# Kernel optimization log

Hardware: AMD Instinct MI355X
Metric: run time of the kernel (lower is better)

The kernel has to match this reference:

```python
import jax, jax.numpy as jnp
import numpy as np

C, CB, W, N = 256, 64, 32, 16
F = CB * W  # 2048 lstm features


def setup_inputs() -> dict:
    key = jax.random.key(0)
    ks = jax.random.split(key, 8)
    sc = 1.0 / np.sqrt(F)  # matches torch LSTM uniform(-1/sqrt(H), 1/sqrt(H)) scale
    return {
        "latent": jax.random.normal(ks[0], (N, C, W, W), jnp.float32),
        "w_in": jax.random.normal(ks[1], (CB, C), jnp.float32) * 0.05,
        "b_in": jnp.zeros((CB,), jnp.float32),
        "w_ih0": jax.random.normal(ks[2], (4 * F, F), jnp.float32) * sc,
        "w_hh0": jax.random.normal(ks[3], (4 * F, F), jnp.float32) * sc,
        "b_ih0": jnp.zeros((4 * F,), jnp.float32),
        "b_hh0": jnp.zeros((4 * F,), jnp.float32),
        "w_ih1": jax.random.normal(ks[4], (4 * F, F), jnp.float32) * sc,
        "w_hh1": jax.random.normal(ks[5], (4 * F, F), jnp.float32) * sc,
        "b_ih1": jnp.zeros((4 * F,), jnp.float32),
        "b_hh1": jnp.zeros((4 * F,), jnp.float32),
        "w_out": jax.random.normal(ks[6], (C, CB), jnp.float32) * 0.05,
        "b_out": jnp.zeros((C,), jnp.float32),
    }


def _lstm_cell(xt, h, c, w_ih, w_hh, b):
    # torch gate order: i, f, g, o
    g = xt @ w_ih.T + h @ w_hh.T + b
    i, f, gg, o = jnp.split(g, 4, axis=-1)
    c = jax.nn.sigmoid(f) * c + jax.nn.sigmoid(i) * jnp.tanh(gg)
    h = jax.nn.sigmoid(o) * jnp.tanh(c)
    return h, c


def reference(latent, w_in, b_in, w_ih0, w_hh0, b_ih0, b_hh0,
              w_ih1, w_hh1, b_ih1, b_hh1, w_out, b_out):
    n, ch, w, hgt = latent.shape
    # bottleneck_in: 1x1 conv (Normalizer.NONE / Activation.NONE -> identity)
    x = jnp.einsum('nchw,oc->nohw', latent, w_in) + b_in[None, :, None, None]  # (N,CB,W,H)
    # (N,CB,W,H) -> (N,W,H,CB) -> (N,W,H*CB) -> (W,N,F)
    seq = x.transpose(0, 2, 3, 1).reshape(n, w, -1).transpose(1, 0, 2)

    b0 = b_ih0 + b_hh0
    b1 = b_ih1 + b_hh1

    def step2(carry, xt):
        h0, c0, h1, c1 = carry
        h0, c0 = _lstm_cell(xt, h0, c0, w_ih0, w_hh0, b0)
        h1, c1 = _lstm_cell(h0, h1, c1, w_ih1, w_hh1, b1)
        return (h0, c0, h1, c1), h1

    z = jnp.zeros((n, seq.shape[-1]), latent.dtype)
    state, outs = jax.lax.scan(step2, (z, z, z, z), seq)
    last = outs[-1]  # out[-1] of full-sequence pass

    def ar_step(carry, _):
        st, xt = carry
        st, y = step2(st, xt)
        return (st, y), y

    _, ar_outs = jax.lax.scan(ar_step, (state, last), None, length=w - 1)
    seq_out = jnp.concatenate([last[None], ar_outs], axis=0)  # (W,N,F)

    # (W,N,F) -> (N,W,F) -> (N,W,H,CB) -> (N,CB,W,H)
    gen = seq_out.transpose(1, 0, 2).reshape(n, w, hgt, -1).transpose(0, 3, 1, 2)
    gen = jnp.einsum('nchw,oc->nohw', gen, w_out) + b_out[None, :, None, None]
    # stitch along spatial W axis (dim=2)
    return jnp.concatenate([latent, gen], axis=2)
```

## Files before the change

kernel.cpp:

```cpp
#include <hip/hip_runtime.h>
#include <hip/hip_bf16.h>

#define NB   16
#define FDIM 2048
#define GDIM 8192
#define WSEQ 32
#define CDIM 256
#define CBD  64
#define HGT  32

#define AGENTSC __HIP_MEMORY_SCOPE_AGENT

typedef float f32x4 __attribute__((ext_vector_type(4)));
typedef long  l64x2 __attribute__((ext_vector_type(2)));
typedef _Float16 f16x4 __attribute__((ext_vector_type(4)));
typedef unsigned char u8;

__device__ __forceinline__ float sigf(float x) { return 1.f / (1.f + __expf(-x)); }

__device__ __forceinline__ u8 f32_to_fp8(float f) {
    int w = __builtin_amdgcn_cvt_pk_fp8_f32(f, f, 0, 0);
    return (u8)(w & 0xff);
}

__global__ __launch_bounds__(256) void pack_w(
        const float* __restrict__ wih0, const float* __restrict__ whh0,
        const float* __restrict__ wih1, const float* __restrict__ whh1,
        u8* __restrict__ W0, u8* __restrict__ W1) {
    __shared__ u8 FW[16][4112];
    int b = blockIdx.x;
    int mat = b >> 9, tile = b & 511;
    const float* wih = mat ? wih1 : wih0;
    const float* whh = mat ? whh1 : whh0;
    int p = tile & 1, jt = tile >> 1;
    int tid = threadIdx.x;
    for (int it = 0; it < 32; it += 4) {
        float4 f[4][2];
#pragma unroll
        for (int r = 0; r < 4; ++r) {
            int c = (it + r) & 15, srcsel = (it + r) >> 4;
            int gate = p * 2 + (c >> 3);
            int rr = gate * FDIM + jt * 8 + (c & 7);
            const float* s = (srcsel ? whh : wih) + (size_t)rr * FDIM + tid * 8;
            f[r][0] = *(const float4*)(s);
            f[r][1] = *(const float4*)(s + 4);
        }
#pragma unroll
        for (int r = 0; r < 4; ++r) {
            int c = (it + r) & 15, srcsel = (it + r) >> 4;
            int w0 = __builtin_amdgcn_cvt_pk_fp8_f32(f[r][0].x, f[r][0].y, 0, 0);
            w0     = __builtin_amdgcn_cvt_pk_fp8_f32(f[r][0].z, f[r][0].w, w0, 1);
            int w1 = __builtin_amdgcn_cvt_pk_fp8_f32(f[r][1].x, f[r][1].y, 0, 0);
            w1     = __builtin_amdgcn_cvt_pk_fp8_f32(f[r][1].z, f[r][1].w, w1, 1);
            *(int2*)&FW[c][srcsel * 2048 + tid * 8] = make_int2(w0, w1);
        }
    }
    __syncthreads();
    u8* base = (mat ? W1 : W0) + (size_t)tile * 65536;
#pragma unroll
    for (int w = 0; w < 16; ++w) {
        int q = w * 256 + tid;
        int kc2 = q >> 6, lane = q & 63;
        int c = lane & 15, kg = lane >> 4;
        l64x2 v;
        v.x = *(const long*)&FW[c][kc2 * 64 + kg * 8];
        v.y = *(const long*)&FW[c][kc2 * 64 + 32 + kg * 8];
        *(l64x2*)(base + (size_t)q * 16) = v;
    }
}

__global__ void bias_k(const float* __restrict__ bih0, const float* __restrict__ bhh0,
                       const float* __restrict__ bih1, const float* __restrict__ bhh1,
                       float* __restrict__ b0, float* __restrict__ b1) {
    int i = blockIdx.x * blockDim.x + threadIdx.x;
    if (i < GDIM)            b0[i] = bih0[i] + bhh0[i];
    else if (i < 2 * GDIM) { int j = i - GDIM; b1[j] = bih1[j] + bhh1[j]; }
}

__global__ __launch_bounds__(256) void conv_in(const float* __restrict__ latent,
                        const float* __restrict__ w_in, const float* __restrict__ b_in,
                        u8* __restrict__ seqbP) {
    __shared__ float lat[CDIM * HGT];
    __shared__ float hv[FDIM];
    int b = blockIdx.x; int n = b >> 5; int t = b & 31;
    int tid = threadIdx.x;
    for (int i = 0; i < 32; ++i) {
        int flat = i * 256 + tid;
        int c = flat >> 5, h = flat & 31;
        lat[flat] = latent[(((size_t)n * CDIM + c) * WSEQ + t) * HGT + h];
    }
    __syncthreads();
    int cb = tid & 63;
    int hb = tid >> 6;
    float acc[8];
#pragma unroll
    for (int k = 0; k < 8; ++k) acc[k] = b_in[cb];
    for (int c = 0; c < CDIM; ++c) {
        float wv = w_in[cb * CDIM + c];
#pragma unroll
        for (int k = 0; k < 8; ++k) acc[k] += lat[c * HGT + (hb + k * 4)] * wv;
    }
#pragma unroll
    for (int k = 0; k < 8; ++k) hv[k * 256 + tid] = acc[k];
    __syncthreads();
    union { u8 by[8]; long l; } pk;
#pragma unroll
    for (int i = 0; i < 8; ++i) pk.by[i] = f32_to_fp8(hv[tid * 8 + i]);
    *(long*)(seqbP + (size_t)t * 32768 + (tid >> 2) * 512 + (tid & 3) * 128 + n * 8) = pk.l;
}

__device__ __forceinline__ void load8_plain(const u8* p, long* f) {
    asm volatile("global_load_dwordx2 %0, %1, off"             : "=v"(f[0]) : "v"(p));
    asm volatile("global_load_dwordx2 %0, %1, off offset:512"  : "=v"(f[1]) : "v"(p));
    asm volatile("global_load_dwordx2 %0, %1, off offset:1024" : "=v"(f[2]) : "v"(p));
    asm volatile("global_load_dwordx2 %0, %1, off offset:1536" : "=v"(f[3]) : "v"(p));
    asm volatile("global_load_dwordx2 %0, %1, off offset:2048" : "=v"(f[4]) : "v"(p));
    asm volatile("global_load_dwordx2 %0, %1, off offset:2560" : "=v"(f[5]) : "v"(p));
    asm volatile("global_load_dwordx2 %0, %1, off offset:3072" : "=v"(f[6]) : "v"(p));
    asm volatile("global_load_dwordx2 %0, %1, off offset:3584" : "=v"(f[7]) : "v"(p));
}

__device__ __forceinline__ void vm_wait0() {
    asm volatile("s_waitcnt vmcnt(0)" ::: "memory");
    __builtin_amdgcn_sched_barrier(0);
}

__device__ __forceinline__ void sync_lds() {
    asm volatile("s_waitcnt lgkmcnt(0)" ::: "memory");
    __builtin_amdgcn_s_barrier();
    asm volatile("" ::: "memory");
}

__device__ __forceinline__ f32x4 mfma8(long a, long b, f32x4 acc) {
    return __builtin_amdgcn_mfma_f32_16x16x32_fp8_fp8(a, b, acc, 0, 0, 0);
}

__device__ __forceinline__ void mma8_reg(const long* f, const l64x2* b, f32x4& acc) {
#pragma unroll
    for (int i = 0; i < 4; ++i) {
        acc = mfma8(f[2 * i],     b[i].x, acc);
        acc = mfma8(f[2 * i + 1], b[i].y, acc);
    }
}
__device__ __forceinline__ void mma8_lds(const long* f, const l64x2* bb, f32x4& acc) {
#pragma unroll
    for (int i = 0; i < 4; ++i) {
        l64x2 bl = bb[(size_t)i * 64];
        acc = mfma8(f[2 * i],     bl.x, acc);
        acc = mfma8(f[2 * i + 1], bl.y, acc);
    }
}

__device__ __forceinline__ void store_frag(_Float16* P, int t, int w,
                                           int kg, int la, f32x4 acc) {
    f16x4 h;
#pragma unroll
    for (int q = 0; q < 4; ++q) h[q] = (_Float16)acc[q];
    *(f16x4*)&P[(((t * 16 + w) * 16) + la) * 16 + kg * 4] = h;
}

__device__ __forceinline__ void cell_tail16(const _Float16* P, int jt, int t2,
        float bi, float bf, float bg, float bo, float& cr,
        u8* hOut, float* seqSlot) {
    int m = t2 >> 3, jj = t2 & 7;
    float gi = 0.f, gf = 0.f, gg = 0.f, go = 0.f;
#pragma unroll
    for (int w2 = 0; w2 < 16; ++w2) {
        int i0 = (w2 * 16 + jj) * 16 + m;
        gi += (float)P[i0];
        gf += (float)P[i0 + 128];
        gg += (float)P[i0 + 4096];
        go += (float)P[i0 + 4224];
    }
    float cn = sigf(gf + bf) * cr + sigf(gi + bi) * tanhf(gg + bg);
    float h  = sigf(go + bo) * tanhf(cn);
    cr = cn;
    u8 hb = f32_to_fp8(h);
    int pos = (jt >> 2) * 512 + (jt & 3) * 128 + t2;
    __hip_atomic_store(hOut + pos, hb, __ATOMIC_RELAXED, AGENTSC);
    if (seqSlot)
        __hip_atomic_store(seqSlot + m * FDIM + jt * 8 + jj, h,
                           __ATOMIC_RELAXED, AGENTSC);
}

__device__ __forceinline__ void grid_bar(unsigned* slots) {
    __syncthreads();
    if (threadIdx.x < 64) {
        if (threadIdx.x == 0) {
            unsigned one = 1u;
            const unsigned* p = slots + blockIdx.x;
            asm volatile("global_store_dword %0, %1, off sc1"
                         :: "v"(p), "v"(one) : "memory");
        }
        const uint4* q = (const uint4*)slots + threadIdx.x;
        int guard = 0;
        while (++guard < (1 << 22)) {
            uint4 v;
            asm volatile("global_load_dwordx4 %0, %1, off sc1"
                         : "=v"(v) : "v"(q) : "memory");
            asm volatile("s_waitcnt vmcnt(0)" ::: "memory");
            if (__all((v.x & v.y & v.z & v.w) != 0u)) break;
            __builtin_amdgcn_s_sleep(1);
        }
    }
    __syncthreads();
}

__global__ __launch_bounds__(1024, 4) void recurrence(
        const u8* __restrict__ W0, const u8* __restrict__ W1,
        const u8* __restrict__ seqbP,
        const float* __restrict__ b0, const float* __restrict__ b1,
        u8* __restrict__ h0buf, u8* __restrict__ h1buf,
        const u8* __restrict__ zb,
        float* __restrict__ sqo, unsigned* __restrict__ arr) {
    __shared__ uint4 w1lds[8192];
    __shared__ _Float16 pA[2 * 16 * 16 * 16];
    __shared__ _Float16 pB[2 * 16 * 16 * 16];
    const int jt = blockIdx.x, tid = threadIdx.x;
    const int w = tid >> 6, l = tid & 63;
    const int la = l & 15, kg = l >> 4;
    {
        const uint4* src = (const uint4*)(W1 + (size_t)jt * 131072);
        for (int i = tid; i < 8192; i += 1024) w1lds[i] = src[i];
    }
    l64x2 w0pin[8];
#pragma unroll
    for (int t = 0; t < 2; ++t)
#pragma unroll
        for (int i = 0; i < 4; ++i)
            w0pin[t * 4 + i] = *(const l64x2*)(W0 +
                ((size_t)((jt * 2 + t) * 64 + w * 4 + i) * 64 + l) * 16);
    float cr = 0.f;
    float bi = 0, bf = 0, bg = 0, bo = 0;
    if (tid < 128) {
        int j = jt * 8 + (tid & 7);
        bi = b0[j]; bf = b0[FDIM + j]; bg = b0[2 * FDIM + j]; bo = b0[3 * FDIM + j];
    } else if (tid < 256) {
        int j = jt * 8 + (tid & 7);
        bi = b1[j]; bf = b1[FDIM + j]; bg = b1[2 * FDIM + j]; bo = b1[3 * FDIM + j];
    }
    __syncthreads();

    unsigned* bs = arr;
    const l64x2* bbA = (const l64x2*)w1lds + ((size_t)(w * 4) * 64 + l);
    const l64x2* bbB = bbA + (size_t)64 * 64;
    const f32x4 z = {0.f, 0.f, 0.f, 0.f};
    const size_t wl = (size_t)w * 4096 + (size_t)l * 8;
    const size_t wh = (size_t)(w - 8) * 4096 + (size_t)l * 8;
#define H0(s) (h0buf + (size_t)(s) * 32768)
#define H1(s) (h1buf + (size_t)(s) * 32768)

    long f0[8], f1[8];

    {
        load8_plain((w < 8) ? seqbP + wl : zb + wh, f0);
        vm_wait0();
        f32x4 t0 = z, t1 = z;
        mma8_reg(f0, w0pin, t0); mma8_reg(f0, w0pin + 4, t1);
        store_frag(pA, 0, w, kg, la, t0);
        store_frag(pA, 1, w, kg, la, t1);
        sync_lds();
        if (tid < 128)
            cell_tail16(pA, jt, tid, bi, bf, bg, bo, cr, H0(0), nullptr);
    }
    for (int s = 0; s <= 30; ++s) {
        if (w < 8) load8_plain(seqbP + (size_t)(s + 1) * 32768 + wl, f0);
        grid_bar(bs); bs += 256;
        if (w >= 8) {
            load8_plain(H0(s) + wh, f0);
            load8_plain((s ? H1(s - 1) : zb) + wh, f1);
        } else {
            load8_plain(H0(s) + wl, f1);
        }
        vm_wait0();
        f32x4 q00 = z, q01 = z, q10 = z, q11 = z;
        mma8_reg(f0, w0pin, q00); mma8_reg(f0, w0pin + 4, q01);
        mma8_lds(f1, bbA, q10);   mma8_lds(f1, bbB, q11);
        store_frag(pA, 0, w, kg, la, q00);
        store_frag(pA, 1, w, kg, la, q01);
        store_frag(pB, 0, w, kg, la, q10);
        store_frag(pB, 1, w, kg, la, q11);
        sync_lds();
        if (tid < 128)
            cell_tail16(pA, jt, tid, bi, bf, bg, bo, cr, H0(s + 1), nullptr);
        else if (tid < 256)
            cell_tail16(pB, jt, tid - 128, bi, bf, bg, bo, cr, H1(s), nullptr);
    }
    {
        grid_bar(bs); bs += 256;
        load8_plain((w < 8) ? H0(31) + wl : H1(30) + wh, f1);
        vm_wait0();
        f32x4 t0 = z, t1 = z;
        mma8_lds(f1, bbA, t0); mma8_lds(f1, bbB, t1);
        if (w >= 8) load8_plain(H0(31) + wh, f0);
        store_frag(pB, 0, w, kg, la, t0);
        store_frag(pB, 1, w, kg, la, t1);
        sync_lds();
        if (tid >= 128 && tid < 256)
            cell_tail16(pB, jt, tid - 128, bi, bf, bg, bo, cr, H1(31), sqo);
    }
    for (int s = 32; s < 63; ++s) {
        grid_bar(bs); bs += 256;
        if (w < 8) load8_plain(H1(s - 1) + wl, f0);
        vm_wait0();
        {
            f32x4 t0 = z, t1 = z;
            mma8_reg(f0, w0pin, t0); mma8_reg(f0, w0pin + 4, t1);
            if (w >= 8) load8_plain(H1(s - 1) + wh, f1);
            store_frag(pA, 0, w, kg, la, t0);
            store_frag(pA, 1, w, kg, la, t1);
            sync_lds();
            if (tid < 128)
                cell_tail16(pA, jt, tid, bi, bf, bg, bo, cr, H0(s), nullptr);
        }
        grid_bar(bs); bs += 256;
        if (w < 8) load8_plain(H0(s) + wl, f1);
        vm_wait0();
        {
            f32x4 t0 = z, t1 = z;
            mma8_lds(f1, bbA, t0); mma8_lds(f1, bbB, t1);
            if (w >= 8 && s != 62) load8_plain(H0(s) + wh, f0);
            store_frag(pB, 0, w, kg, la, t0);
            store_frag(pB, 1, w, kg, la, t1);
            sync_lds();
            if (tid >= 128 && tid < 256)
                cell_tail16(pB, jt, tid - 128, bi, bf, bg, bo, cr, H1(s),
                            sqo + (size_t)(s - 31) * NB * FDIM);
        }
    }
#undef H0
#undef H1
}

__global__ void copy_lat(const float* __restrict__ latent, float* __restrict__ out) {
    size_t i = (size_t)blockIdx.x * blockDim.x + threadIdx.x;
    if (i >= (size_t)1048576) return;
    size_t blk = i >> 8;
    size_t within = i & 255;
    float4 v = ((const float4*)latent)[i];
    ((float4*)out)[blk * 512 + within] = v;
}

__global__ __launch_bounds__(256) void gen_out(const float* __restrict__ seq_out,
                        const float* __restrict__ w_out, const float* __restrict__ b_out,
                        float* __restrict__ out) {
    __shared__ float row[32 * 65];
    int b = blockIdx.x; int n = b >> 5, t = b & 31;
    const float* src = seq_out + ((size_t)t * NB + n) * FDIM;
    for (int i = threadIdx.x; i < FDIM; i += 256)
        row[(i >> 6) * 65 + (i & 63)] = src[i];
    __syncthreads();
    for (int it = 0; it < 32; ++it) {
        int o = it * 256 + threadIdx.x;
        int c = o >> 5, h = o & 31;
        float acc = b_out[c];
#pragma unroll
        for (int cb = 0; cb < CBD; ++cb) acc += row[h * 65 + cb] * w_out[c * CBD + cb];
        out[(((size_t)n * CDIM + c) * 64 + 32 + t) * HGT + h] = acc;
    }
}

extern "C" void kernel_launch(void* const* d_in, const int* in_sizes, int n_in,
                              void* d_out, int out_size, void* d_ws, size_t ws_size,
                              hipStream_t stream) {
    const float* latent = (const float*)d_in[0];
    const float* w_in   = (const float*)d_in[1];
    const float* b_in   = (const float*)d_in[2];
    const float* w_ih0  = (const float*)d_in[3];
    const float* w_hh0  = (const float*)d_in[4];
    const float* b_ih0  = (const float*)d_in[5];
    const float* b_hh0  = (const float*)d_in[6];
    const float* w_ih1  = (const float*)d_in[7];
    const float* w_hh1  = (const float*)d_in[8];
    const float* b_ih1  = (const float*)d_in[9];
    const float* b_hh1  = (const float*)d_in[10];
    const float* w_out  = (const float*)d_in[11];
    const float* b_out  = (const float*)d_in[12];
    float* out = (float*)d_out;
    char* ws = (char*)d_ws;

    size_t off = 0;
    u8*    W0   = (u8*)(ws + off); off += (size_t)512 * 65536;
    u8*    W1   = (u8*)(ws + off); off += (size_t)512 * 65536;
    u8*    seqbP= (u8*)(ws + off); off += (size_t)WSEQ * 32768;
    float* sqo  = (float*)(ws + off); off += (size_t)WSEQ * NB * FDIM * 4;
    u8*    h0buf= (u8*)(ws + off); off += (size_t)64 * 32768;
    u8*    h1buf= (u8*)(ws + off); off += (size_t)64 * 32768;
    char*  zbase = ws + off;
    u8*    zb   = (u8*)(ws + off); off += 32768;
    unsigned* arr = (unsigned*)(ws + off); off += (size_t)96 * 1024;
    size_t zbytes = (size_t)(ws + off - zbase);
    float* b0 = (float*)(ws + off); off += (size_t)GDIM * 4;
    float* b1 = (float*)(ws + off); off += (size_t)GDIM * 4;

    if (ws_size < off) {
        hipMemsetAsync(d_out, 0, (size_t)out_size * 4, stream);
        return;
    }

    hipMemsetAsync(zbase, 0, zbytes, stream);
    pack_w<<<1024, 256, 0, stream>>>(w_ih0, w_hh0, w_ih1, w_hh1, W0, W1);
    bias_k<<<64, 256, 0, stream>>>(b_ih0, b_hh0, b_ih1, b_hh1, b0, b1);
    conv_in<<<512, 256, 0, stream>>>(latent, w_in, b_in, seqbP);
    recurrence<<<256, 1024, 0, stream>>>(W0, W1, seqbP, b0, b1,
                                         h0buf, h1buf, zb, sqo, arr);
    copy_lat<<<4096, 256, 0, stream>>>(latent, out);
    gen_out<<<512, 256, 0, stream>>>(sqo, w_out, b_out, out);
}
```

Measured before the change: 809.7 us.

## Halve recurrence block size, give each wave twice the K-chunk, pad partial-sum LDS

The persistent LSTM recurrence kernel now runs 512-thread blocks (8 waves) instead of 1024, and each wave covers a K-chunk twice as long with 16 fp8 MFMAs per accumulator. Pinned W0 registers and load buffers double. The cross-wave partial-sum reduction in the cell tail shrinks from 16 to 8 terms, and the LDS layout gets a padded stride of 20 to reduce bank conflicts. In the layer-0+1 overlap phase, a split vmcnt wait lets the input-projection MFMAs start before the hidden-state loads land. This cuts barrier and reduction cost per step, at the price of higher register pressure and fewer waves to hide latency.

```diff
diff --git a/kernel.cpp b/kernel.cpp
--- a/kernel.cpp
+++ b/kernel.cpp
@@ -119,9 +119,17 @@
     asm volatile("global_load_dwordx2 %0, %1, off offset:3072" : "=v"(f[6]) : "v"(p));
     asm volatile("global_load_dwordx2 %0, %1, off offset:3584" : "=v"(f[7]) : "v"(p));
 }
+__device__ __forceinline__ void load16_plain(const u8* p, long* f) {
+    load8_plain(p, f);
+    load8_plain(p + 4096, f + 8);
+}
 
 __device__ __forceinline__ void vm_wait0() {
     asm volatile("s_waitcnt vmcnt(0)" ::: "memory");
+    __builtin_amdgcn_sched_barrier(0);
+}
+__device__ __forceinline__ void vm_wait16() {
+    asm volatile("s_waitcnt vmcnt(16)" ::: "memory");
     __builtin_amdgcn_sched_barrier(0);
 }
 
@@ -135,16 +143,16 @@
     return __builtin_amdgcn_mfma_f32_16x16x32_fp8_fp8(a, b, acc, 0, 0, 0);
 }
 
-__device__ __forceinline__ void mma8_reg(const long* f, const l64x2* b, f32x4& acc) {
-#pragma unroll
-    for (int i = 0; i < 4; ++i) {
+__device__ __forceinline__ void mma16_reg(const long* f, const l64x2* b, f32x4& acc) {
+#pragma unroll
+    for (int i = 0; i < 8; ++i) {
         acc = mfma8(f[2 * i],     b[i].x, acc);
         acc = mfma8(f[2 * i + 1], b[i].y, acc);
     }
 }
-__device__ __forceinline__ void mma8_lds(const long* f, const l64x2* bb, f32x4& acc) {
-#pragma unroll
-    for (int i = 0; i < 4; ++i) {
+__device__ __forceinline__ void mma16_lds(const long* f, const l64x2* bb, f32x4& acc) {
+#pragma unroll
+    for (int i = 0; i < 8; ++i) {
         l64x2 bl = bb[(size_t)i * 64];
         acc = mfma8(f[2 * i],     bl.x, acc);
         acc = mfma8(f[2 * i + 1], bl.y, acc);
@@ -156,21 +164,21 @@
     f16x4 h;
 #pragma unroll
     for (int q = 0; q < 4; ++q) h[q] = (_Float16)acc[q];
-    *(f16x4*)&P[(((t * 16 + w) * 16) + la) * 16 + kg * 4] = h;
-}
-
-__device__ __forceinline__ void cell_tail16(const _Float16* P, int jt, int t2,
+    *(f16x4*)&P[(((t * 8 + w) * 16) + la) * 20 + kg * 4] = h;
+}
+
+__device__ __forceinline__ void cell_tail8(const _Float16* P, int jt, int t2,
         float bi, float bf, float bg, float bo, float& cr,
         u8* hOut, float* seqSlot) {
     int m = t2 >> 3, jj = t2 & 7;
     float gi = 0.f, gf = 0.f, gg = 0.f, go = 0.f;
 #pragma unroll
-    for (int w2 = 0; w2 < 16; ++w2) {
-        int i0 = (w2 * 16 + jj) * 16 + m;
+    for (int w2 = 0; w2 < 8; ++w2) {
+        int i0 = (w2 * 16 + jj) * 20 + m;
         gi += (float)P[i0];
-        gf += (float)P[i0 + 128];
-        gg += (float)P[i0 + 4096];
-        go += (float)P[i0 + 4224];
+        gf += (float)P[i0 + 160];
+        gg += (float)P[i0 + 2560];
+        go += (float)P[i0 + 2720];
     }
     float cn = sigf(gf + bf) * cr + sigf(gi + bi) * tanhf(gg + bg);
     float h  = sigf(go + bo) * tanhf(cn);
@@ -206,7 +214,7 @@
     __syncthreads();
 }
 
-__global__ __launch_bounds__(1024, 4) void recurrence(
+__global__ __launch_bounds__(512, 2) void recurrence(
         const u8* __restrict__ W0, const u8* __restrict__ W1,
         const u8* __restrict__ seqbP,
         const float* __restrict__ b0, const float* __restrict__ b1,
@@ -214,22 +222,22 @@
         const u8* __restrict__ zb,
         float* __restrict__ sqo, unsigned* __restrict__ arr) {
     __shared__ uint4 w1lds[8192];
-    __shared__ _Float16 pA[2 * 16 * 16 * 16];
-    __shared__ _Float16 pB[2 * 16 * 16 * 16];
+    __shared__ _Float16 pA[2 * 8 * 16 * 20];
+    __shared__ _Float16 pB[2 * 8 * 16 * 20];
     const int jt = blockIdx.x, tid = threadIdx.x;
     const int w = tid >> 6, l = tid & 63;
     const int la = l & 15, kg = l >> 4;
     {
         const uint4* src = (const uint4*)(W1 + (size_t)jt * 131072);
-        for (int i = tid; i < 8192; i += 1024) w1lds[i] = src[i];
-    }
-    l64x2 w0pin[8];
+        for (int i = tid; i < 8192; i += 512) w1lds[i] = src[i];
+    }
+    l64x2 w0pin[16];
 #pragma unroll
     for (int t = 0; t < 2; ++t)
 #pragma unroll
-        for (int i = 0; i < 4; ++i)
-            w0pin[t * 4 + i] = *(const l64x2*)(W0 +
-                ((size_t)((jt * 2 + t) * 64 + w * 4 + i) * 64 + l) * 16);
+        for (int i = 0; i < 8; ++i)
+            w0pin[t * 8 + i] = *(const l64x2*)(W0 +
+                ((size_t)((jt * 2 + t) * 64 + w * 8 + i) * 64 + l) * 16);
     float cr = 0.f;
     float bi = 0, bf = 0, bg = 0, bo = 0;
     if (tid < 128) {
@@ -242,90 +250,91 @@
     __syncthreads();
 
     unsigned* bs = arr;
-    const l64x2* bbA = (const l64x2*)w1lds + ((size_t)(w * 4) * 64 + l);
+    const l64x2* bbA = (const l64x2*)w1lds + ((size_t)(w * 8) * 64 + l);
     const l64x2* bbB = bbA + (size_t)64 * 64;
     const f32x4 z = {0.f, 0.f, 0.f, 0.f};
-    const size_t wl = (size_t)w * 4096 + (size_t)l * 8;
-    const size_t wh = (size_t)(w - 8) * 4096 + (size_t)l * 8;
+    const size_t wl = (size_t)w * 8192 + (size_t)l * 8;
+    const size_t wh = (size_t)(w - 4) * 8192 + (size_t)l * 8;
 #define H0(s) (h0buf + (size_t)(s) * 32768)
 #define H1(s) (h1buf + (size_t)(s) * 32768)
 
-    long f0[8], f1[8];
+    long f0[16], f1[16];
 
     {
-        load8_plain((w < 8) ? seqbP + wl : zb + wh, f0);
+        load16_plain((w < 4) ? seqbP + wl : zb + wh, f0);
         vm_wait0();
         f32x4 t0 = z, t1 = z;
-        mma8_reg(f0, w0pin, t0); mma8_reg(f0, w0pin + 4, t1);
+        mma16_reg(f0, w0pin, t0); mma16_reg(f0, w0pin + 8, t1);
         store_frag(pA, 0, w, kg, la, t0);
         store_frag(pA, 1, w, kg, la, t1);
         sync_lds();
         if (tid < 128)
-            cell_tail16(pA, jt, tid, bi, bf, bg, bo, cr, H0(0), nullptr);
+            cell_tail8(pA, jt, tid, bi, bf, bg, bo, cr, H0(0), nullptr);
     }
     for (int s = 0; s <= 30; ++s) {
-        if (w < 8) load8_plain(seqbP + (size_t)(s + 1) * 32768 + wl, f0);
+        if (w < 4) load16_plain(seqbP + (size_t)(s + 1) * 32768 + wl, f0);
         grid_bar(bs); bs += 256;
-        if (w >= 8) {
-            load8_plain(H0(s) + wh, f0);
-            load8_plain((s ? H1(s - 1) : zb) + wh, f1);
+        if (w >= 4) {
+            load16_plain(H0(s) + wh, f0);
+            load16_plain((s ? H1(s - 1) : zb) + wh, f1);
         } else {
-            load8_plain(H0(s) + wl, f1);
-        }
+            load16_plain(H0(s) + wl, f1);
+        }
+        vm_wait16();
+        f32x4 q00 = z, q01 = z, q10 = z, q11 = z;
+        mma16_reg(f0, w0pin, q00); mma16_reg(f0, w0pin + 8, q01);
         vm_wait0();
-        f32x4 q00 = z, q01 = z, q10 = z, q11 = z;
-        mma8_reg(f0, w0pin, q00); mma8_reg(f0, w0pin + 4, q01);
-        mma8_lds(f1, bbA, q10);   mma8_lds(f1, bbB, q11);
+        mma16_lds(f1, bbA, q10);   mma16_lds(f1, bbB, q11);
         store_frag(pA, 0, w, kg, la, q00);
         store_frag(pA, 1, w, kg, la, q01);
         store_frag(pB, 0, w, kg, la, q10);
         store_frag(pB, 1, w, kg, la, q11);
         sync_lds();
         if (tid < 128)
-            cell_tail16(pA, jt, tid, bi, bf, bg, bo, cr, H0(s + 1), nullptr);
+            cell_tail8(pA, jt, tid, bi, bf, bg, bo, cr, H0(s + 1), nullptr);
         else if (tid < 256)
-            cell_tail16(pB, jt, tid - 128, bi, bf, bg, bo, cr, H1(s), nullptr);
+            cell_tail8(pB, jt, tid - 128, bi, bf, bg, bo, cr, H1(s), nullptr);
     }
     {
         grid_bar(bs); bs += 256;
-        load8_plain((w < 8) ? H0(31) + wl : H1(30) + wh, f1);
+        load16_plain((w < 4) ? H0(31) + wl : H1(30) + wh, f1);
         vm_wait0();
         f32x4 t0 = z, t1 = z;
-        mma8_lds(f1, bbA, t0); mma8_lds(f1, bbB, t1);
-        if (w >= 8) load8_plain(H0(31) + wh, f0);
+        mma16_lds(f1, bbA, t0); mma16_lds(f1, bbB, t1);
+        if (w >= 4) load16_plain(H0(31) + wh, f0);
         store_frag(pB, 0, w, kg, la, t0);
         store_frag(pB, 1, w, kg, la, t1);
         sync_lds();
         if (tid >= 128 && tid < 256)
-            cell_tail16(pB, jt, tid - 128, bi, bf, bg, bo, cr, H1(31), sqo);
+            cell_tail8(pB, jt, tid - 128, bi, bf, bg, bo, cr, H1(31), sqo);
     }
     for (int s = 32; s < 63; ++s) {
         grid_bar(bs); bs += 256;
-        if (w < 8) load8_plain(H1(s - 1) + wl, f0);
+        if (w < 4) load16_plain(H1(s - 1) + wl, f0);
         vm_wait0();
         {
             f32x4 t0 = z, t1 = z;
-            mma8_reg(f0, w0pin, t0); mma8_reg(f0, w0pin + 4, t1);
-            if (w >= 8) load8_plain(H1(s - 1) + wh, f1);
+            mma16_reg(f0, w0pin, t0); mma16_reg(f0, w0pin + 8, t1);
+            if (w >= 4) load16_plain(H1(s - 1) + wh, f1);
             store_frag(pA, 0, w, kg, la, t0);
             store_frag(pA, 1, w, kg, la, t1);
             sync_lds();
             if (tid < 128)
-                cell_tail16(pA, jt, tid, bi, bf, bg, bo, cr, H0(s), nullptr);
+                cell_tail8(pA, jt, tid, bi, bf, bg, bo, cr, H0(s), nullptr);
         }
         grid_bar(bs); bs += 256;
-        if (w < 8) load8_plain(H0(s) + wl, f1);
+        if (w < 4) load16_plain(H0(s) + wl, f1);
         vm_wait0();
         {
             f32x4 t0 = z, t1 = z;
-            mma8_lds(f1, bbA, t0); mma8_lds(f1, bbB, t1);
-            if (w >= 8 && s != 62) load8_plain(H0(s) + wh, f0);
+            mma16_lds(f1, bbA, t0); mma16_lds(f1, bbB, t1);
+            if (w >= 4 && s != 62) load16_plain(H0(s) + wh, f0);
             store_frag(pB, 0, w, kg, la, t0);
             store_frag(pB, 1, w, kg, la, t1);
             sync_lds();
             if (tid >= 128 && tid < 256)
-                cell_tail16(pB, jt, tid - 128, bi, bf, bg, bo, cr, H1(s),
-                            sqo + (size_t)(s - 31) * NB * FDIM);
+                cell_tail8(pB, jt, tid - 128, bi, bf, bg, bo, cr, H1(s),
+                           sqo + (size_t)(s - 31) * NB * FDIM);
         }
     }
 #undef H0
@@ -402,8 +411,8 @@
     pack_w<<<1024, 256, 0, stream>>>(w_ih0, w_hh0, w_ih1, w_hh1, W0, W1);
     bias_k<<<64, 256, 0, stream>>>(b_ih0, b_hh0, b_ih1, b_hh1, b0, b1);
     conv_in<<<512, 256, 0, stream>>>(latent, w_in, b_in, seqbP);
-    recurrence<<<256, 1024, 0, stream>>>(W0, W1, seqbP, b0, b1,
-                                         h0buf, h1buf, zb, sqo, arr);
+    recurrence<<<256, 512, 0, stream>>>(W0, W1, seqbP, b0, b1,
+                                        h0buf, h1buf, zb, sqo, arr);
     copy_lat<<<4096, 256, 0, stream>>>(latent, out);
     gen_out<<<512, 256, 0, stream>>>(sqo, w_out, b_out, out);
 }
```

Result: faster. 700.1 us (-13.5%).
